# Optimization experiments

Measured on AMD Instinct MI355X. Metric: run time of the kernel, lower is better.

The kernel has to match this reference:

```python
import jax, jax.numpy as jnp
import numpy as np

RCR, RCA = 5.1, 3.5
ETA_R, ZETA, ETA_A = 19.7, 14.1, 12.5
SHF_R = jnp.asarray((0.8 + 0.26875 * np.arange(16)).astype(np.float32))   # 16 radial shifts
SHF_Z = jnp.asarray(((2 * np.arange(8) + 1) * np.pi / 8).astype(np.float32))  # 8 angle shifts
SHF_A = jnp.asarray((0.8 + 0.3375 * np.arange(8)).astype(np.float32))    # 8 angular-radial shifts
NUM_SPECIES = 7
NUM_PAIRS = NUM_SPECIES * (NUM_SPECIES + 1) // 2  # 28 unordered species pairs
N = 2000          # atoms
K = 24            # max neighbors considered for angular terms (Rca=3.5 -> ~18 at this density)
BOX = 27.1        # (N / 0.1 atoms/A^3)^(1/3)

def _triu_index(n):
    ret = np.zeros((n, n), dtype=np.int32)
    iu = np.triu_indices(n)
    ret[iu] = np.arange(iu[0].size)
    ret[iu[1], iu[0]] = ret[iu]
    return ret
TRIU = jnp.asarray(_triu_index(NUM_SPECIES))  # [7,7] -> pair index in 0..27

def _fc(d, rc):
    # cosine cutoff, zero beyond rc
    return jnp.where(d <= rc, 0.5 * jnp.cos(jnp.pi * d / rc) + 0.5, 0.0)

def setup_inputs():
    key = jax.random.key(0)
    k1, k2 = jax.random.split(key)
    species = jax.random.randint(k1, (N,), 0, NUM_SPECIES)
    positions = jax.random.uniform(k2, (N, 3), dtype=jnp.float32) * BOX
    return {"species": species, "positions": positions}

def _aev_mean(species, positions):
    n = positions.shape[0]
    eye = jnp.eye(n, dtype=bool)
    diff = positions[:, None, :] - positions[None, :, :]          # [n,n,3]
    d2 = jnp.sum(diff * diff, -1)
    dist = jnp.sqrt(jnp.where(eye, 1.0, d2))                      # safe sqrt on diagonal
    dist = jnp.where(eye, 2.0 * RCR, dist)                        # exclude self (fc -> 0)

    # ---- radial AEV: 0.25 * exp(-EtaR (d - ShfR)^2) * fc(d, Rcr), scattered by neighbor species
    fc_r = _fc(dist, RCR)
    rad = 0.25 * jnp.exp(-ETA_R * (dist[..., None] - SHF_R) ** 2) * fc_r[..., None]  # [n,n,16]
    oh = jax.nn.one_hot(species, NUM_SPECIES, dtype=positions.dtype)                  # [n,7]
    radial = jnp.einsum('ijr,js->isr', rad, oh)                   # [n,7,16]

    # ---- angular AEV over triplets (j, i, k) with j,k among K nearest neighbors of i
    neg, idx = jax.lax.top_k(-dist, K)                            # idx: [n,K]
    nd = -neg                                                     # neighbor distances [n,K]
    valid = nd <= RCA
    vec = positions[idx] - positions[:, None, :]                  # [n,K,3]
    rj = nd[:, :, None]
    rk = nd[:, None, :]
    cos_ang = 0.95 * jnp.einsum('nad,nbd->nab', vec, vec) / (rj * rk)  # torchani's 0.95 factor
    theta = jnp.arccos(cos_ang)                                   # [n,K,K]
    f1 = ((1.0 + jnp.cos(theta[..., None] - SHF_Z)) / 2.0) ** ZETA               # [n,K,K,8]
    f2 = jnp.exp(-ETA_A * (((rj + rk) / 2.0)[..., None] - SHF_A) ** 2)           # [n,K,K,8]
    fcj = _fc(nd, RCA)
    tri = jnp.triu(jnp.ones((K, K), dtype=bool), 1)               # unordered pairs j<k
    mask = valid[:, :, None] & valid[:, None, :] & tri
    pref = 2.0 * fcj[:, :, None] * fcj[:, None, :] * mask.astype(positions.dtype)
    g = (f1[..., :, None] * f2[..., None, :]).reshape(n, K, K, 64) * pref[..., None]  # [n,K,K,64]
    sp_nb = species[idx]                                          # [n,K]
    pair_idx = TRIU[sp_nb[:, :, None], sp_nb[:, None, :]]         # [n,K,K] in 0..27
    row = jnp.arange(n)[:, None, None]
    angular = jnp.zeros((n, NUM_PAIRS, 64), dtype=positions.dtype).at[row, pair_idx].add(g)

    aev = jnp.concatenate([radial.reshape(n, -1), angular.reshape(n, -1)], axis=-1)  # [n,1904]
    return jnp.mean(aev)

def reference(species, positions):
    return _aev_mean(species, positions)
```

## Files before the change

kernel.cpp:

```cpp
#include <hip/hip_runtime.h>
#include <math.h>

#define NATOMS   2000
#define KNBR     24
#define HCAP     192
#define ACAP     64
#define BLOCK    256
#define NFEAT    1904.0f

__device__ __forceinline__ float wave_reduce_add(float v) {
    #pragma unroll
    for (int off = 32; off > 0; off >>= 1) v += __shfl_down(v, off, 64);
    return v;
}

__global__ __launch_bounds__(BLOCK) void aev_block_kernel(
        const float* __restrict__ pos, float* __restrict__ partial) {
    constexpr float RCR = 5.1f, RCA = 3.5f;
    constexpr float ETA_R = 19.7f, ZETA = 14.1f, ETA_A = 12.5f;
    constexpr float PI = 3.14159265358979323846f;

    __shared__ float hd2[HCAP];
    __shared__ int   hj[HCAP];
    __shared__ float ad[ACAP];
    __shared__ int   aj[ACAP];
    __shared__ int   s_hcnt, s_acnt;
    __shared__ float nbx[KNBR], nby[KNBR], nbz[KNBR], nbd[KNBR], nbfc[KNBR];
    __shared__ float red[BLOCK / 64];

    const int tid  = threadIdx.x;
    const int i    = blockIdx.x;
    const int lane = tid & 63;

    if (tid == 0) { s_hcnt = 0; s_acnt = 0; }
    __syncthreads();

    const float xi = pos[3 * i + 0], yi = pos[3 * i + 1], zi = pos[3 * i + 2];

    for (int jb = 0; jb < NATOMS; jb += BLOCK) {
        int j  = jb + tid;
        int jc = j < NATOMS ? j : NATOMS - 1;
        float dx = pos[3 * jc + 0] - xi;
        float dy = pos[3 * jc + 1] - yi;
        float dz = pos[3 * jc + 2] - zi;
        float d2 = dx * dx + dy * dy + dz * dz;
        bool hit = (j < NATOMS) && (j != i) && (d2 <= RCR * RCR);
        unsigned long long m = __ballot(hit);
        int nw   = __popcll(m);
        int base = 0;
        if (lane == 0 && nw) base = atomicAdd(&s_hcnt, nw);
        base = __shfl(base, 0, 64);
        if (hit) {
            int idx = base + __popcll(m & ((1ull << lane) - 1ull));
            if (idx < HCAP) { hd2[idx] = d2; hj[idx] = j; }
        }
    }
    __syncthreads();

    float psum = 0.0f;
    int hcnt = min(s_hcnt, HCAP);
    for (int c = tid; c < hcnt; c += BLOCK) {
        float d2 = hd2[c];
        float d  = sqrtf(d2);
        float fc = 0.5f * __cosf(d * (PI / RCR)) + 0.5f;
        float s  = 0.0f;
        #pragma unroll
        for (int r = 0; r < 16; r++) {
            float t = d - (0.8f + 0.26875f * (float)r);
            s += __expf(-ETA_R * t * t);
        }
        psum += 0.25f * fc * s;
        if (d2 <= RCA * RCA) {
            int a = atomicAdd(&s_acnt, 1);
            if (a < ACAP) { ad[a] = d; aj[a] = hj[c]; }
        }
    }
    __syncthreads();

    int cnt = min(s_acnt, ACAP);
    int M   = min(cnt, KNBR);
    if (tid < cnt) {
        float dt = ad[tid];
        int   jt = aj[tid];
        int rank = 0;
        for (int u = 0; u < cnt; u++) {
            float du = ad[u];
            if (du < dt || (du == dt && aj[u] < jt)) rank++;
        }
        if (rank < KNBR) {
            nbx[rank]  = pos[3 * jt + 0] - xi;
            nby[rank]  = pos[3 * jt + 1] - yi;
            nbz[rank]  = pos[3 * jt + 2] - zi;
            nbd[rank]  = dt;
            nbfc[rank] = 0.5f * __cosf(dt * (PI / RCA)) + 0.5f;
        }
    }
    __syncthreads();

    int npairs = M * (M - 1) / 2;
    for (int p = tid; p < npairs; p += BLOCK) {
        int a = 0, rem = p;
        while (rem >= M - 1 - a) { rem -= M - 1 - a; a++; }
        int b = a + 1 + rem;

        float dot = nbx[a] * nbx[b] + nby[a] * nby[b] + nbz[a] * nbz[b];
        float ra = nbd[a], rb = nbd[b];
        float cosang = 0.95f * dot / (ra * rb);
        float theta  = acosf(cosang);

        float f1 = 0.0f;
        #pragma unroll
        for (int z = 0; z < 8; z++) {
            float shz = (2.0f * (float)z + 1.0f) * (PI / 8.0f);
            float c   = 0.5f * (1.0f + __cosf(theta - shz));
            f1 += __powf(fmaxf(c, 1e-20f), ZETA);
        }
        float avg = 0.5f * (ra + rb);
        float f2  = 0.0f;
        #pragma unroll
        for (int s8 = 0; s8 < 8; s8++) {
            float t = avg - (0.8f + 0.3375f * (float)s8);
            f2 += __expf(-ETA_A * t * t);
        }
        psum += 2.0f * nbfc[a] * nbfc[b] * f1 * f2;
    }

    psum = wave_reduce_add(psum);
    if (lane == 0) red[tid >> 6] = psum;
    __syncthreads();
    if (tid == 0) {
        float total = 0.0f;
        #pragma unroll
        for (int w = 0; w < BLOCK / 64; w++) total += red[w];
        partial[i] = total;
    }
}

__global__ __launch_bounds__(BLOCK) void finalize_kernel(
        const float* __restrict__ partial, float* __restrict__ out) {
    __shared__ float red[BLOCK / 64];
    const int tid = threadIdx.x;
    float v = 0.0f;
    for (int c = tid; c < NATOMS; c += BLOCK) v += partial[c];
    v = wave_reduce_add(v);
    if ((tid & 63) == 0) red[tid >> 6] = v;
    __syncthreads();
    if (tid == 0) {
        float total = 0.0f;
        #pragma unroll
        for (int w = 0; w < BLOCK / 64; w++) total += red[w];
        out[0] = total / ((float)NATOMS * NFEAT);
    }
}

extern "C" void kernel_launch(void* const* d_in, const int* in_sizes, int n_in,
                              void* d_out, int out_size, void* d_ws, size_t ws_size,
                              hipStream_t stream) {
    const float* pos = (const float*)d_in[1];
    float* partial = (float*)d_ws;

    aev_block_kernel<<<NATOMS, BLOCK, 0, stream>>>(pos, partial);
    finalize_kernel<<<1, BLOCK, 0, stream>>>(partial, (float*)d_out);
}
```

Measured before the change: 78.62 us.

## Use per-wave neighbor lists and replace acos/cos with angle-addition identity

The block-wide shared atomic counters for neighbor compaction become per-wave lists built with ballot and mbcnt, so each wave handles its own 512-atom strided slice without LDS atomics. The radial terms are computed directly by the wave that found the neighbors, and one block barrier is dropped. The angular term no longer calls acosf and eight cosines: it uses cos(theta - shift) = ca*cos(shift) + sa*sin(shift), and since the shifts come in symmetric pairs, four products serve all eight terms. The trade-off is hard per-wave caps (48 radial, 24 angular), which could silently drop neighbors if the local density runs high.

```diff
diff --git a/kernel.cpp b/kernel.cpp
--- a/kernel.cpp
+++ b/kernel.cpp
@@ -1,17 +1,23 @@
 #include <hip/hip_runtime.h>
 #include <math.h>
 
-#define NATOMS   2000
-#define KNBR     24
-#define HCAP     192
-#define ACAP     64
-#define BLOCK    256
-#define NFEAT    1904.0f
+#define NATOMS 2000
+#define KNBR   24
+#define BLOCK  256
+#define NWAVE  4
+#define WHCAP  48
+#define WACAP  24
+#define NFEAT  1904.0f
 
 __device__ __forceinline__ float wave_reduce_add(float v) {
     #pragma unroll
     for (int off = 32; off > 0; off >>= 1) v += __shfl_down(v, off, 64);
     return v;
+}
+
+__device__ __forceinline__ int mask_rank_below(unsigned long long m) {
+    return (int)__builtin_amdgcn_mbcnt_hi((unsigned)(m >> 32),
+                 __builtin_amdgcn_mbcnt_lo((unsigned)m, 0u));
 }
 
 __global__ __launch_bounds__(BLOCK) void aev_block_kernel(
@@ -20,72 +26,84 @@
     constexpr float ETA_R = 19.7f, ZETA = 14.1f, ETA_A = 12.5f;
     constexpr float PI = 3.14159265358979323846f;
 
-    __shared__ float hd2[HCAP];
-    __shared__ int   hj[HCAP];
-    __shared__ float ad[ACAP];
-    __shared__ int   aj[ACAP];
-    __shared__ int   s_hcnt, s_acnt;
+    __shared__ float hd2[NWAVE][WHCAP];
+    __shared__ int   hj [NWAVE][WHCAP];
+    __shared__ float ad [NWAVE][WACAP];
+    __shared__ int   aj [NWAVE][WACAP];
+    __shared__ int   acnt[NWAVE];
     __shared__ float nbx[KNBR], nby[KNBR], nbz[KNBR], nbd[KNBR], nbfc[KNBR];
-    __shared__ float red[BLOCK / 64];
+    __shared__ float red[NWAVE];
 
     const int tid  = threadIdx.x;
+    const int w    = tid >> 6;
+    const int lane = tid & 63;
     const int i    = blockIdx.x;
-    const int lane = tid & 63;
-
-    if (tid == 0) { s_hcnt = 0; s_acnt = 0; }
-    __syncthreads();
 
     const float xi = pos[3 * i + 0], yi = pos[3 * i + 1], zi = pos[3 * i + 2];
 
-    for (int jb = 0; jb < NATOMS; jb += BLOCK) {
-        int j  = jb + tid;
-        int jc = j < NATOMS ? j : NATOMS - 1;
+    int hbase = 0;
+    #pragma unroll 4
+    for (int it = 0; it < 8; it++) {
+        int j  = w * 64 + it * 256 + lane;
+        int jc = j < NATOMS ? j : 0;
         float dx = pos[3 * jc + 0] - xi;
         float dy = pos[3 * jc + 1] - yi;
         float dz = pos[3 * jc + 2] - zi;
         float d2 = dx * dx + dy * dy + dz * dz;
         bool hit = (j < NATOMS) && (j != i) && (d2 <= RCR * RCR);
         unsigned long long m = __ballot(hit);
-        int nw   = __popcll(m);
-        int base = 0;
-        if (lane == 0 && nw) base = atomicAdd(&s_hcnt, nw);
-        base = __shfl(base, 0, 64);
         if (hit) {
-            int idx = base + __popcll(m & ((1ull << lane) - 1ull));
-            if (idx < HCAP) { hd2[idx] = d2; hj[idx] = j; }
+            int idx = hbase + mask_rank_below(m);
+            if (idx < WHCAP) { hd2[w][idx] = d2; hj[w][idx] = j; }
         }
+        hbase += __popcll(m);
+    }
+
+    int hcnt = min(hbase, WHCAP);
+    float rsum = 0.0f;
+    float d = 0.0f, d2v = 1e9f;
+    bool act = lane < hcnt;
+    {
+        int cl = min(lane, WHCAP - 1);
+        if (act) d2v = hd2[w][cl];
+        if (act) {
+            d = sqrtf(d2v);
+            float fc = 0.5f * __cosf(d * (PI / RCR)) + 0.5f;
+            float s = 0.0f;
+            #pragma unroll
+            for (int r = 0; r < 16; r++) {
+                float t = d - (0.8f + 0.26875f * (float)r);
+                s += __expf(-ETA_R * t * t);
+            }
+            rsum = 0.25f * fc * s;
+        }
+        bool ahit = act && (d2v <= RCA * RCA);
+        unsigned long long m = __ballot(ahit);
+        if (ahit) {
+            int idx = mask_rank_below(m);
+            if (idx < WACAP) { ad[w][idx] = d; aj[w][idx] = hj[w][min(lane, WHCAP - 1)]; }
+        }
+        if (lane == 0) acnt[w] = min((int)__popcll(m), WACAP);
     }
     __syncthreads();
 
-    float psum = 0.0f;
-    int hcnt = min(s_hcnt, HCAP);
-    for (int c = tid; c < hcnt; c += BLOCK) {
-        float d2 = hd2[c];
-        float d  = sqrtf(d2);
-        float fc = 0.5f * __cosf(d * (PI / RCR)) + 0.5f;
-        float s  = 0.0f;
-        #pragma unroll
-        for (int r = 0; r < 16; r++) {
-            float t = d - (0.8f + 0.26875f * (float)r);
-            s += __expf(-ETA_R * t * t);
-        }
-        psum += 0.25f * fc * s;
-        if (d2 <= RCA * RCA) {
-            int a = atomicAdd(&s_acnt, 1);
-            if (a < ACAP) { ad[a] = d; aj[a] = hj[c]; }
-        }
-    }
-    __syncthreads();
-
-    int cnt = min(s_acnt, ACAP);
+    int c0 = acnt[0], c1 = acnt[1], c2 = acnt[2], c3 = acnt[3];
+    int cnt = min(c0 + c1 + c2 + c3, 64);
     int M   = min(cnt, KNBR);
     if (tid < cnt) {
-        float dt = ad[tid];
-        int   jt = aj[tid];
+        int t = tid, seg = 0;
+        if (t >= c0) { t -= c0; seg = 1;
+            if (t >= c1) { t -= c1; seg = 2;
+                if (t >= c2) { t -= c2; seg = 3; } } }
+        float dt = ad[seg][t];
+        int   jt = aj[seg][t];
         int rank = 0;
-        for (int u = 0; u < cnt; u++) {
-            float du = ad[u];
-            if (du < dt || (du == dt && aj[u] < jt)) rank++;
+        for (int s = 0; s < NWAVE; s++) {
+            int cs = acnt[s];
+            for (int u = 0; u < cs; u++) {
+                float du = ad[s][u];
+                if (du < dt || (du == dt && aj[s][u] < jt)) rank++;
+            }
         }
         if (rank < KNBR) {
             nbx[rank]  = pos[3 * jt + 0] - xi;
@@ -97,23 +115,26 @@
     }
     __syncthreads();
 
+    const float CZ[4] = { 0.92387953251f, 0.38268343236f, -0.38268343236f, -0.92387953251f };
+    const float SZ[4] = { 0.38268343236f, 0.92387953251f,  0.92387953251f,  0.38268343236f };
+    float asum = 0.0f;
     int npairs = M * (M - 1) / 2;
     for (int p = tid; p < npairs; p += BLOCK) {
         int a = 0, rem = p;
         while (rem >= M - 1 - a) { rem -= M - 1 - a; a++; }
         int b = a + 1 + rem;
 
+        float ra = nbd[a], rb = nbd[b];
         float dot = nbx[a] * nbx[b] + nby[a] * nby[b] + nbz[a] * nbz[b];
-        float ra = nbd[a], rb = nbd[b];
-        float cosang = 0.95f * dot / (ra * rb);
-        float theta  = acosf(cosang);
+        float ca = 0.95f * dot / (ra * rb);
+        float sa = sqrtf(fmaxf(0.0f, 1.0f - ca * ca));
 
         float f1 = 0.0f;
         #pragma unroll
-        for (int z = 0; z < 8; z++) {
-            float shz = (2.0f * (float)z + 1.0f) * (PI / 8.0f);
-            float c   = 0.5f * (1.0f + __cosf(theta - shz));
-            f1 += __powf(fmaxf(c, 1e-20f), ZETA);
+        for (int z = 0; z < 4; z++) {
+            float g = 0.5f * (ca * CZ[z] + sa * SZ[z]);
+            f1 += __powf(fmaxf(0.5f + g, 1e-20f), ZETA);
+            f1 += __powf(fmaxf(0.5f - g, 1e-20f), ZETA);
         }
         float avg = 0.5f * (ra + rb);
         float f2  = 0.0f;
@@ -122,16 +143,16 @@
             float t = avg - (0.8f + 0.3375f * (float)s8);
             f2 += __expf(-ETA_A * t * t);
         }
-        psum += 2.0f * nbfc[a] * nbfc[b] * f1 * f2;
+        asum += 2.0f * nbfc[a] * nbfc[b] * f1 * f2;
     }
 
-    psum = wave_reduce_add(psum);
-    if (lane == 0) red[tid >> 6] = psum;
+    float psum = wave_reduce_add(rsum + asum);
+    if (lane == 0) red[w] = psum;
     __syncthreads();
     if (tid == 0) {
         float total = 0.0f;
         #pragma unroll
-        for (int w = 0; w < BLOCK / 64; w++) total += red[w];
+        for (int q = 0; q < NWAVE; q++) total += red[q];
         partial[i] = total;
     }
 }
@@ -148,7 +169,7 @@
     if (tid == 0) {
         float total = 0.0f;
         #pragma unroll
-        for (int w = 0; w < BLOCK / 64; w++) total += red[w];
+        for (int q = 0; q < BLOCK / 64; q++) total += red[q];
         out[0] = total / ((float)NATOMS * NFEAT);
     }
 }
```

Measured after the change: 79.87 us. No clear change (+1.6%).
